# Kernel optimization log

Measured on AMD Instinct MI355X. Metric: run time of the kernel, lower is better.

The kernel has to match this reference:

```python
import jax, jax.numpy as jnp
import numpy as np

MARGIN = 0.3
ANCHOR = 0.5
EPS = 1e-8  # torch F.cosine_similarity default eps


def _cosine(a, b):
    # a: [N, D], b: [D] -> [N]
    num = a @ b
    den = jnp.maximum(jnp.linalg.norm(a, axis=-1) * jnp.linalg.norm(b), EPS)
    return num / den


def setup_inputs() -> dict:
    key = jax.random.key(0)
    k1, k2, k3, k4 = jax.random.split(key, 4)
    N, D = 8192, 1024
    return {
        "q_emb": jax.random.normal(k1, (D,), dtype=jnp.float32),
        "d_embs": jax.random.normal(k2, (N, D), dtype=jnp.float32),
        "c_emb": jax.random.normal(k3, (D,), dtype=jnp.float32),
        "rates": jax.random.uniform(k4, (N,), dtype=jnp.float32),
    }


def reference(q_emb, d_embs, c_emb, rates):
    # cosine similarity of each distractor vs question / correct answer
    s_q = _cosine(d_embs, q_emb)          # [N]
    _s_c = _cosine(d_embs, c_emb)         # [N] computed in original, never used
    quality = jnp.abs(rates - ANCHOR)     # [N]

    # Vectorized form of the nested i,j loop:
    # pair (i, j) contributes relu(margin + s_q[j] - s_q[i]) iff quality[i] > quality[j]
    mask = quality[:, None] > quality[None, :]              # [N, N]; diagonal is False
    pair_loss = jax.nn.relu(MARGIN + s_q[None, :] - s_q[:, None])  # [N, N]
    total = jnp.sum(jnp.where(mask, pair_loss, jnp.float32(0.0)))
    n_pairs = jnp.sum(mask)
    return total / jnp.maximum(n_pairs, 1).astype(total.dtype)
```

## Files before the change

### kernel.cpp

```cpp
#include <hip/hip_runtime.h>

#define MARGIN 0.3f
#define ANCHOR 0.5f
#define EPS    1e-8f
#define BJ     256

typedef unsigned long long ull;

__global__ __launch_bounds__(256) void sq_kernel(
        const float* __restrict__ q, const float* __restrict__ d,
        const float* __restrict__ rates,
        float* __restrict__ sq, float* __restrict__ qual,
        int N, int D) {
    int wave = (blockIdx.x * blockDim.x + threadIdx.x) >> 6;
    int lane = threadIdx.x & 63;
    if (wave >= N) return;
    const float* row = d + (size_t)wave * (size_t)D;

    float dot = 0.f, dn = 0.f, qn = 0.f;
    for (int it = lane * 4; it < D; it += 256) {
        float4 dv = *(const float4*)(row + it);
        float4 qv = *(const float4*)(q + it);
        dot += dv.x * qv.x + dv.y * qv.y + dv.z * qv.z + dv.w * qv.w;
        dn  += dv.x * dv.x + dv.y * dv.y + dv.z * dv.z + dv.w * dv.w;
        qn  += qv.x * qv.x + qv.y * qv.y + qv.z * qv.z + qv.w * qv.w;
    }
    #pragma unroll
    for (int off = 32; off >= 1; off >>= 1) {
        dot += __shfl_xor(dot, off);
        dn  += __shfl_xor(dn,  off);
        qn  += __shfl_xor(qn,  off);
    }
    if (lane == 0) {
        float den = fmaxf(sqrtf(dn) * sqrtf(qn), EPS);
        sq[wave]   = dot / den;
        qual[wave] = fabsf(rates[wave] - ANCHOR);
    }
}

__global__ __launch_bounds__(256) void pair_kernel(
        const float* __restrict__ sq, const float* __restrict__ qual,
        int N, double* __restrict__ psum, unsigned* __restrict__ pcnt) {
    __shared__ float2 tile[BJ];

    int tid = threadIdx.x;
    int i   = blockIdx.x * blockDim.x + tid;
    int j0  = blockIdx.y * BJ;

    if (tid < BJ) {
        int j = j0 + tid;
        tile[tid] = make_float2(j < N ? sq[j] : 0.f,
                                j < N ? qual[j] : 1e30f);
    }
    __syncthreads();

    float my_sq = (i < N) ? sq[i]   : 0.f;
    float my_q  = (i < N) ? qual[i] : -1.f;
    float a     = MARGIN - my_sq;

    float sum = 0.f;
    unsigned c = 0;
    #pragma unroll 8
    for (int j = 0; j < BJ; ++j) {
        float2 t = tile[j];
        bool  m = my_q > t.y;
        float v = fmaxf(a + t.x, 0.f);
        sum += m ? v : 0.f;
        c   += m ? 1u : 0u;
    }

    #pragma unroll
    for (int off = 32; off >= 1; off >>= 1) {
        sum += __shfl_xor(sum, off);
        c   += __shfl_xor(c,   off);
    }
    __shared__ double   bsum[4];
    __shared__ unsigned bcnt[4];
    int w = tid >> 6;
    if ((tid & 63) == 0) { bsum[w] = (double)sum; bcnt[w] = c; }
    __syncthreads();
    if (tid == 0) {
        int bid = blockIdx.y * gridDim.x + blockIdx.x;
        psum[bid] = bsum[0] + bsum[1] + bsum[2] + bsum[3];
        pcnt[bid] = bcnt[0] + bcnt[1] + bcnt[2] + bcnt[3];
    }
}

__global__ __launch_bounds__(256) void reduce_kernel(
        const double* __restrict__ psum, const unsigned* __restrict__ pcnt,
        int nb, float* __restrict__ out) {
    int tid = threadIdx.x;
    double s = 0.0;
    ull    c = 0ull;
    for (int k = tid; k < nb; k += 256) {
        s += psum[k];
        c += (ull)pcnt[k];
    }
    #pragma unroll
    for (int off = 32; off >= 1; off >>= 1) {
        s += __shfl_xor(s, off);
        c += __shfl_xor(c, off);
    }
    __shared__ double bsum[4];
    __shared__ ull    bcnt[4];
    int w = tid >> 6;
    if ((tid & 63) == 0) { bsum[w] = s; bcnt[w] = c; }
    __syncthreads();
    if (tid == 0) {
        double T = bsum[0] + bsum[1] + bsum[2] + bsum[3];
        ull    C = bcnt[0] + bcnt[1] + bcnt[2] + bcnt[3];
        if (C < 1ull) C = 1ull;
        out[0] = (float)(T / (double)C);
    }
}

extern "C" void kernel_launch(void* const* d_in, const int* in_sizes, int n_in,
                              void* d_out, int out_size, void* d_ws, size_t ws_size,
                              hipStream_t stream) {
    const float* q_emb  = (const float*)d_in[0];
    const float* d_embs = (const float*)d_in[1];
    const float* rates  = (const float*)d_in[3];

    int D = in_sizes[0];
    int N = in_sizes[3];

    dim3 grid((N + 255) / 256, (N + BJ - 1) / BJ);
    int  nb = grid.x * grid.y;

    double*   psum = (double*)d_ws;
    unsigned* pcnt = (unsigned*)(psum + nb);
    float*    sq   = (float*)(pcnt + nb + (nb & 1));
    float*    qual = sq + N;
    float*    out  = (float*)d_out;

    int rows_per_block = 256 / 64;
    sq_kernel<<<(N + rows_per_block - 1) / rows_per_block, 256, 0, stream>>>(
        q_emb, d_embs, rates, sq, qual, N, D);

    pair_kernel<<<grid, 256, 0, stream>>>(sq, qual, N, psum, pcnt);

    reduce_kernel<<<1, 256, 0, stream>>>(psum, pcnt, nb, out);
}
```

Measured before the change: 24.65 us.

## Fuse final reduction into pair kernel via slotted atomics and last-block detection

Drops the separate single-block reduce kernel. Each pair block atomically adds its partial sum and count into one of 32 padded slots, and the last block to finish reads the slots and writes the mean. The accumulators are zeroed inside sq_kernel, which saves a kernel launch and the write and read of per-block partials. In exchange it adds atomic contention and a memory-ordering dependence between the atomics and the final read.

```diff
diff --git a/kernel.cpp b/kernel.cpp
--- a/kernel.cpp
+++ b/kernel.cpp
@@ -4,16 +4,25 @@
 #define ANCHOR 0.5f
 #define EPS    1e-8f
 #define BJ     256
+#define NSLOT  32
 
 typedef unsigned long long ull;
+
 
 __global__ __launch_bounds__(256) void sq_kernel(
         const float* __restrict__ q, const float* __restrict__ d,
         const float* __restrict__ rates,
         float* __restrict__ sq, float* __restrict__ qual,
-        int N, int D) {
-    int wave = (blockIdx.x * blockDim.x + threadIdx.x) >> 6;
-    int lane = threadIdx.x & 63;
+        char* __restrict__ acc, int N, int D) {
+    int tid = threadIdx.x;
+    if (blockIdx.x == 0) {
+        if (tid < NSLOT)              *(double*)  (acc + (size_t)tid * 64)              = 0.0;
+        else if (tid < 2 * NSLOT)     *(unsigned*)(acc + 2048 + (size_t)(tid - 32) * 64) = 0u;
+        else if (tid < 3 * NSLOT)     *(unsigned*)(acc + 4096 + (size_t)(tid - 64) * 64) = 0u;
+        else if (tid == 3 * NSLOT)    *(unsigned*)(acc + 6144)                           = 0u;
+    }
+    int wave = (blockIdx.x * blockDim.x + tid) >> 6;
+    int lane = tid & 63;
     if (wave >= N) return;
     const float* row = d + (size_t)wave * (size_t)D;
 
@@ -40,8 +49,10 @@
 
 __global__ __launch_bounds__(256) void pair_kernel(
         const float* __restrict__ sq, const float* __restrict__ qual,
-        int N, double* __restrict__ psum, unsigned* __restrict__ pcnt) {
-    __shared__ float2 tile[BJ];
+        int N, char* __restrict__ acc, float* __restrict__ out, unsigned nblocks) {
+    __shared__ float2   tile[BJ];
+    __shared__ double   bsum[4];
+    __shared__ unsigned bcnt[4];
 
     int tid = threadIdx.x;
     int i   = blockIdx.x * blockDim.x + tid;
@@ -49,7 +60,7 @@
 
     if (tid < BJ) {
         int j = j0 + tid;
-        tile[tid] = make_float2(j < N ? sq[j] : 0.f,
+        tile[tid] = make_float2(j < N ? sq[j]   : 0.f,
                                 j < N ? qual[j] : 1e30f);
     }
     __syncthreads();
@@ -74,43 +85,48 @@
         sum += __shfl_xor(sum, off);
         c   += __shfl_xor(c,   off);
     }
-    __shared__ double   bsum[4];
-    __shared__ unsigned bcnt[4];
     int w = tid >> 6;
     if ((tid & 63) == 0) { bsum[w] = (double)sum; bcnt[w] = c; }
     __syncthreads();
+
+    if (tid >= 64) return;
+
+    unsigned last = 0;
     if (tid == 0) {
-        int bid = blockIdx.y * gridDim.x + blockIdx.x;
-        psum[bid] = bsum[0] + bsum[1] + bsum[2] + bsum[3];
-        pcnt[bid] = bcnt[0] + bcnt[1] + bcnt[2] + bcnt[3];
+        double   bs = bsum[0] + bsum[1] + bsum[2] + bsum[3];
+        unsigned bc = bcnt[0] + bcnt[1] + bcnt[2] + bcnt[3];
+        unsigned bid = blockIdx.y * gridDim.x + blockIdx.x;
+        unsigned s   = bid & (NSLOT - 1);
+
+        double   old  = atomicAdd((double*)  (acc + (size_t)s * 64), bs);
+        unsigned oldc = atomicAdd((unsigned*)(acc + 2048 + (size_t)s * 64), bc);
+        asm volatile("" :: "v"(__double2hiint(old)), "v"(__double2loint(old)), "v"(oldc));
+
+        unsigned gsz = (nblocks > s) ? ((nblocks - 1u - s) / NSLOT + 1u) : 0u;
+        unsigned pa  = atomicAdd((unsigned*)(acc + 4096 + (size_t)s * 64), 1u);
+        if (pa == gsz - 1u) {
+            asm volatile("" :: "v"(pa));
+            unsigned nslots = (nblocks < NSLOT) ? nblocks : NSLOT;
+            unsigned pm = atomicAdd((unsigned*)(acc + 6144), 1u);
+            last = (pm == nslots - 1u) ? 1u : 0u;
+        }
     }
-}
-
-__global__ __launch_bounds__(256) void reduce_kernel(
-        const double* __restrict__ psum, const unsigned* __restrict__ pcnt,
-        int nb, float* __restrict__ out) {
-    int tid = threadIdx.x;
-    double s = 0.0;
-    ull    c = 0ull;
-    for (int k = tid; k < nb; k += 256) {
-        s += psum[k];
-        c += (ull)pcnt[k];
-    }
-    #pragma unroll
-    for (int off = 32; off >= 1; off >>= 1) {
-        s += __shfl_xor(s, off);
-        c += __shfl_xor(c, off);
-    }
-    __shared__ double bsum[4];
-    __shared__ ull    bcnt[4];
-    int w = tid >> 6;
-    if ((tid & 63) == 0) { bsum[w] = s; bcnt[w] = c; }
-    __syncthreads();
-    if (tid == 0) {
-        double T = bsum[0] + bsum[1] + bsum[2] + bsum[3];
-        ull    C = bcnt[0] + bcnt[1] + bcnt[2] + bcnt[3];
-        if (C < 1ull) C = 1ull;
-        out[0] = (float)(T / (double)C);
+    last = __shfl(last, 0);
+    if (last) {
+        double s = 0.0; ull c2 = 0ull;
+        if (tid < NSLOT) {
+            s  = atomicAdd((double*)  (acc + (size_t)tid * 64), 0.0);
+            c2 = (ull)atomicAdd((unsigned*)(acc + 2048 + (size_t)tid * 64), 0u);
+        }
+        #pragma unroll
+        for (int off = 16; off >= 1; off >>= 1) {
+            s  += __shfl_xor(s,  off);
+            c2 += __shfl_xor(c2, off);
+        }
+        if (tid == 0) {
+            if (c2 < 1ull) c2 = 1ull;
+            out[0] = (float)(s / (double)c2);
+        }
     }
 }
 
@@ -124,20 +140,16 @@
     int D = in_sizes[0];
     int N = in_sizes[3];
 
-    dim3 grid((N + 255) / 256, (N + BJ - 1) / BJ);
-    int  nb = grid.x * grid.y;
-
-    double*   psum = (double*)d_ws;
-    unsigned* pcnt = (unsigned*)(psum + nb);
-    float*    sq   = (float*)(pcnt + nb + (nb & 1));
-    float*    qual = sq + N;
-    float*    out  = (float*)d_out;
+    char*  acc  = (char*)d_ws;
+    float* sq   = (float*)(acc + 8192);
+    float* qual = sq + N;
+    float* out  = (float*)d_out;
 
     int rows_per_block = 256 / 64;
     sq_kernel<<<(N + rows_per_block - 1) / rows_per_block, 256, 0, stream>>>(
-        q_emb, d_embs, rates, sq, qual, N, D);
+        q_emb, d_embs, rates, sq, qual, acc, N, D);
 
-    pair_kernel<<<grid, 256, 0, stream>>>(sq, qual, N, psum, pcnt);
-
-    reduce_kernel<<<1, 256, 0, stream>>>(psum, pcnt, nb, out);
+    dim3 grid((N + 255) / 256, (N + BJ - 1) / BJ);
+    pair_kernel<<<grid, 256, 0, stream>>>(sq, qual, N, acc, out,
+                                          grid.x * grid.y);
 }
```

After: 23.75 us. 1.04x faster.
